# Kernel tuning notes

Hardware: AMD Instinct MI355X
Metric: run time of the kernel (lower is better)

Reference implementation:

```python
import jax, jax.numpy as jnp
import numpy as np

B, T, N_EMBD, HEAD = 4, 2048, 1024, 128


def setup_inputs() -> dict:
    key = jax.random.key(0)
    ks = jax.random.split(key, 7)
    s = 1.0 / np.sqrt(N_EMBD)
    return {
        "X": jax.random.normal(ks[0], (B, T, N_EMBD), dtype=jnp.float32),
        "Wk": jax.random.normal(ks[1], (N_EMBD, HEAD), dtype=jnp.float32) * s,
        "bk": jax.random.normal(ks[2], (HEAD,), dtype=jnp.float32) * 0.02,
        "Wq": jax.random.normal(ks[3], (N_EMBD, HEAD), dtype=jnp.float32) * s,
        "bq": jax.random.normal(ks[4], (HEAD,), dtype=jnp.float32) * 0.02,
        "Wv": jax.random.normal(ks[5], (N_EMBD, HEAD), dtype=jnp.float32) * s,
        "bv": jax.random.normal(ks[6], (HEAD,), dtype=jnp.float32) * 0.02,
    }


def reference(X, Wk, bk, Wq, bq, Wv, bv):
    # X: [B, T, C] with C = n_embd
    C = X.shape[-1]
    k = X @ Wk + bk  # [B, T, H]
    q = X @ Wq + bq  # [B, T, H]
    # NOTE: original computes k @ q^T (not q @ k^T) and scales by n_embd**-0.5.
    wei = jnp.einsum("bth,bsh->bts", k, q) * (C ** -0.5)  # [B, T, T]
    # NOTE: original's masked_fill is not in-place and its result is discarded,
    # so NO causal mask is actually applied. Dropout is identity (eval).
    wei = jax.nn.softmax(wei, axis=-1)
    v = X @ Wv + bv  # [B, T, H]
    out = jnp.einsum("bts,bsh->bth", wei, v)  # [B, T, H]
    return out
```

## Files before the change

kernel.cpp:

```cpp
#include <hip/hip_runtime.h>
#include <hip/hip_bf16.h>

#define Bn 4
#define Tn 2048
#define Cn 1024
#define Hn 128
#define Mn (Bn*Tn)
#define SCHUNKS 4
#define SCHUNK  (Tn/SCHUNKS)

typedef _Float16 f16;
typedef __attribute__((ext_vector_type(4))) _Float16 f16x4;
typedef __attribute__((ext_vector_type(8))) _Float16 f16x8;
typedef __attribute__((ext_vector_type(4))) float f32x4;

__global__ void prep_w(const float* __restrict__ Wk, const float* __restrict__ Wq,
                       const float* __restrict__ Wv, f16* __restrict__ Wt) {
    const int w = blockIdx.y;
    const float* W = (w == 0) ? Wk : (w == 1) ? Wq : Wv;
    int idx = blockIdx.x * 256 + threadIdx.x;
    int c = idx >> 7;
    int h = idx & 127;
    Wt[w * (Cn * Hn) + h * Cn + c] = (f16)W[idx];
}

__global__ __launch_bounds__(512) void qkv_gemm(const float* __restrict__ X,
                                                const f16* __restrict__ Wt,
                                                const float* __restrict__ bk,
                                                const float* __restrict__ bq,
                                                const float* __restrict__ bv,
                                                f16* __restrict__ proj) {
    __shared__ __align__(16) f16 As[32 * 72];
    __shared__ __align__(16) f16 Bs[384 * 72];

    const int tid  = threadIdx.x;
    const int r0   = blockIdx.x * 32;
    const int lane = tid & 63, wid = tid >> 6;
    const int quad = lane >> 4, l16 = lane & 15;
    const int nbase = wid * 48;

    f32x4 acc[2][3] = {};

    for (int k0 = 0; k0 < Cn; k0 += 64) {
        {
            int row = tid >> 4, c4 = tid & 15;
            float4 x = *(const float4*)(X + (r0 + row) * Cn + k0 + c4 * 4);
            f16x4 v = { (f16)x.x, (f16)x.y, (f16)x.z, (f16)x.w };
            *(f16x4*)(&As[row * 72 + c4 * 4]) = v;
        }
        for (int i = 0; i < 6; i++) {
            int ci = tid + 512 * i;
            int row = ci >> 3, cc = ci & 7;
            *(f16x8*)(&Bs[row * 72 + cc * 8]) =
                *(const f16x8*)(Wt + row * Cn + k0 + cc * 8);
        }
        __syncthreads();
        for (int ks = 0; ks < 2; ks++) {
            int kk = ks * 32;
            f16x8 af[2], bf[3];
            for (int mt = 0; mt < 2; mt++)
                af[mt] = *(const f16x8*)(&As[(mt * 16 + l16) * 72 + kk + quad * 8]);
            for (int nt = 0; nt < 3; nt++)
                bf[nt] = *(const f16x8*)(&Bs[(nbase + nt * 16 + l16) * 72 + kk + quad * 8]);
            for (int mt = 0; mt < 2; mt++)
                for (int nt = 0; nt < 3; nt++)
                    acc[mt][nt] = __builtin_amdgcn_mfma_f32_16x16x32_f16(
                        af[mt], bf[nt], acc[mt][nt], 0, 0, 0);
        }
        __syncthreads();
    }

    for (int nt = 0; nt < 3; nt++) {
        int n0 = nbase + nt * 16;
        int wsel = n0 >> 7;
        int col = (n0 & 127) + l16;
        const float* bias = (wsel == 0) ? bk : (wsel == 1) ? bq : bv;
        float bval = bias[col];
        float scale = (wsel == 0) ? 0.03125f : 1.0f;
        f16* P = proj + wsel * (Mn * Hn);
        for (int mt = 0; mt < 2; mt++)
            for (int r = 0; r < 4; r++) {
                int m = r0 + mt * 16 + quad * 4 + r;
                P[m * Hn + col] = (f16)((acc[mt][nt][r] + bval) * scale);
            }
    }
}

__global__ __launch_bounds__(256) void vt_transpose(const f16* __restrict__ pv,
                                                    f16* __restrict__ vT) {
    __shared__ __align__(16) f16 T[64 * 72];
    const int tid = threadIdx.x;
    const int s0 = blockIdx.x * 64, h0 = blockIdx.y * 64, b = blockIdx.z;
    for (int i = 0; i < 2; i++) {
        int ci = tid + 256 * i;
        int row = ci >> 3, hc = ci & 7;
        *(f16x8*)(&T[row * 72 + hc * 8]) =
            *(const f16x8*)(pv + (b * Tn + s0 + row) * Hn + h0 + hc * 8);
    }
    __syncthreads();
    for (int i = 0; i < 2; i++) {
        int ci = tid + 256 * i;
        int h = ci >> 3, sc = ci & 7;
        f16x8 v;
        for (int j = 0; j < 8; j++) v[j] = T[(sc * 8 + j) * 72 + h];
        *(f16x8*)(&vT[(b * Hn + h0 + h) * Tn + s0 + sc * 8]) = v;
    }
}

__global__ __launch_bounds__(256) void attn_kernel(const f16* __restrict__ pk,
                                                   const f16* __restrict__ pq,
                                                   const f16* __restrict__ vT,
                                                   float* __restrict__ pO,
                                                   float* __restrict__ pm,
                                                   float* __restrict__ pl) {
    __shared__ __align__(16) char smem[36864];
    f16* Bq = (f16*)smem;
    f16* Vt = (f16*)(smem + 17408);

    const int tid  = threadIdx.x;
    const int tblk = blockIdx.x, c = blockIdx.y, b = blockIdx.z;
    const int t0   = tblk * 64;
    const int lane = tid & 63, wid = tid >> 6;
    const int quad = lane >> 4, l16 = lane & 15;
    const int tg   = t0 + wid * 16 + l16;

    const f16* kp = pk + b * Tn * Hn;
    const f16* qp = pq + b * Tn * Hn;
    const f16* vp = vT + b * Hn * Tn;

    f16x8 kfr[4];
    for (int ks = 0; ks < 4; ks++)
        kfr[ks] = *(const f16x8*)(kp + tg * Hn + ks * 32 + quad * 8);

    float m_i = -3e38f, l_i = 0.0f;
    f32x4 accO[8] = {};

    for (int si = 0; si < SCHUNK / 64; si++) {
        const int s0 = c * SCHUNK + si * 64;
        for (int i = 0; i < 4; i++) {
            int ci = tid + 256 * i;
            int row = ci >> 4, hc = ci & 15;
            *(f16x8*)(&Bq[row * 136 + hc * 8]) =
                *(const f16x8*)(qp + (s0 + row) * Hn + hc * 8);
        }
        for (int i = 0; i < 4; i++) {
            int ci = tid + 256 * i;
            int h = ci >> 3, sc = ci & 7;
            *(f16x8*)(&Vt[h * 72 + sc * 8]) =
                *(const f16x8*)(vp + h * Tn + s0 + sc * 8);
        }
        __syncthreads();

        f32x4 accS[4] = {};
        for (int ks = 0; ks < 4; ks++) {
            int kk = ks * 32;
            for (int st = 0; st < 4; st++) {
                f16x8 af = *(const f16x8*)(&Bq[(st * 16 + l16) * 136 + kk + quad * 8]);
                accS[st] = __builtin_amdgcn_mfma_f32_16x16x32_f16(af, kfr[ks], accS[st], 0, 0, 0);
            }
        }

        float mloc = -3e38f;
        for (int st = 0; st < 4; st++)
            for (int r = 0; r < 4; r++) mloc = fmaxf(mloc, accS[st][r]);
        mloc = fmaxf(mloc, __shfl_xor(mloc, 16));
        mloc = fmaxf(mloc, __shfl_xor(mloc, 32));
        float mnew = fmaxf(m_i, mloc);
        float alpha = __expf(m_i - mnew);
        m_i = mnew;

        f16x4 pf[4];
        float psum = 0.0f;
        for (int st = 0; st < 4; st++) {
            f32x4 p;
            for (int r = 0; r < 4; r++) {
                p[r] = __expf(accS[st][r] - mnew);
                psum += p[r];
            }
            pf[st] = { (f16)p[0], (f16)p[1], (f16)p[2], (f16)p[3] };
        }
        psum += __shfl_xor(psum, 16);
        psum += __shfl_xor(psum, 32);
        l_i = l_i * alpha + psum;

        for (int ht = 0; ht < 8; ht++)
            for (int r = 0; r < 4; r++) accO[ht][r] *= alpha;

        for (int st = 0; st < 4; st++) {
            for (int ht = 0; ht < 8; ht++) {
                f16x4 av = *(const f16x4*)(&Vt[(ht * 16 + l16) * 72 + st * 16 + quad * 4]);
                accO[ht] = __builtin_amdgcn_mfma_f32_16x16x16f16(av, pf[st], accO[ht], 0, 0, 0);
            }
        }
        __syncthreads();
    }

    float* ep = (float*)smem + wid * 2048;
    for (int ht = 0; ht < 8; ht++)
        for (int r = 0; r < 4; r++)
            ep[(ht * 16 + quad * 4 + r) * 16 + l16] = accO[ht][r];
    __syncthreads();
    {
        int t = lane >> 2, hq = lane & 3;
        int tgl = t0 + wid * 16 + t;
        float* dst = pO + ((size_t)(c * Bn + b) * Tn + tgl) * Hn + hq * 32;
        for (int j = 0; j < 8; j++) {
            float4 v = { ep[(hq * 32 + j * 4 + 0) * 16 + t],
                         ep[(hq * 32 + j * 4 + 1) * 16 + t],
                         ep[(hq * 32 + j * 4 + 2) * 16 + t],
                         ep[(hq * 32 + j * 4 + 3) * 16 + t] };
            *(float4*)(dst + j * 4) = v;
        }
    }
    if (quad == 0) {
        pm[(c * Bn + b) * Tn + t0 + wid * 16 + l16] = m_i;
        pl[(c * Bn + b) * Tn + t0 + wid * 16 + l16] = l_i;
    }
}

__global__ __launch_bounds__(256) void merge_kernel(const float* __restrict__ pO,
                                                    const float* __restrict__ pm,
                                                    const float* __restrict__ pl,
                                                    float* __restrict__ out) {
    int gid = blockIdx.x * 256 + threadIdx.x;
    int tg = gid >> 2;
    int hq = gid & 3;
    float mc[SCHUNKS], lc[SCHUNKS];
    float M = -3e38f;
    for (int cI = 0; cI < SCHUNKS; cI++) {
        mc[cI] = pm[cI * (Bn * Tn) + tg];
        lc[cI] = pl[cI * (Bn * Tn) + tg];
        M = fmaxf(M, mc[cI]);
    }
    float L = 0.0f, wc[SCHUNKS];
    for (int cI = 0; cI < SCHUNKS; cI++) {
        wc[cI] = __expf(mc[cI] - M);
        L += wc[cI] * lc[cI];
    }
    float inv = 1.0f / L;
    float4 o[8] = {};
    for (int cI = 0; cI < SCHUNKS; cI++) {
        const float* src = pO + ((size_t)cI * Bn * Tn + tg) * Hn + hq * 32;
        float w = wc[cI];
        for (int j = 0; j < 8; j++) {
            float4 v = *(const float4*)(src + j * 4);
            o[j].x += w * v.x; o[j].y += w * v.y; o[j].z += w * v.z; o[j].w += w * v.w;
        }
    }
    float* dst = out + (size_t)tg * Hn + hq * 32;
    for (int j = 0; j < 8; j++) {
        float4 v = { o[j].x * inv, o[j].y * inv, o[j].z * inv, o[j].w * inv };
        *(float4*)(dst + j * 4) = v;
    }
}

extern "C" void kernel_launch(void* const* d_in, const int* in_sizes, int n_in,
                              void* d_out, int out_size, void* d_ws, size_t ws_size,
                              hipStream_t stream) {
    const float* X  = (const float*)d_in[0];
    const float* Wk = (const float*)d_in[1];
    const float* bk = (const float*)d_in[2];
    const float* Wq = (const float*)d_in[3];
    const float* bq = (const float*)d_in[4];
    const float* Wv = (const float*)d_in[5];
    const float* bv = (const float*)d_in[6];
    float* out = (float*)d_out;

    char* base = (char*)d_ws;
    f16*   Wt   = (f16*)(base);
    f16*   proj = (f16*)(base + 786432);
    f16*   pk   = proj;
    f16*   pq   = proj + Mn * Hn;
    f16*   pv   = proj + 2 * Mn * Hn;
    f16*   vT   = (f16*)(base + 7077888);
    float* pO   = (float*)(base + 9175040);
    float* pm   = (float*)(base + 25952256);
    float* pl   = (float*)(base + 26083328);

    prep_w<<<dim3(512, 3), 256, 0, stream>>>(Wk, Wq, Wv, Wt);
    qkv_gemm<<<dim3(Mn / 32), 512, 0, stream>>>(X, Wt, bk, bq, bv, proj);
    vt_transpose<<<dim3(Tn / 64, Hn / 64, Bn), 256, 0, stream>>>(pv, vT);
    attn_kernel<<<dim3(Tn / 64, SCHUNKS, Bn), 256, 0, stream>>>(pk, pq, vT, pO, pm, pl);
    merge_kernel<<<dim3(128), 256, 0, stream>>>(pO, pm, pl, out);
}
```

Measured before the change: 146.2 us.

## Double per-wave row tile in attention, split S into 8 chunks, store partials as fp16

```diff
diff --git a/kernel.cpp b/kernel.cpp
--- a/kernel.cpp
+++ b/kernel.cpp
@@ -6,7 +6,7 @@
 #define Cn 1024
 #define Hn 128
 #define Mn (Bn*Tn)
-#define SCHUNKS 4
+#define SCHUNKS 8
 #define SCHUNK  (Tn/SCHUNKS)
 
 typedef _Float16 f16;
@@ -107,33 +107,34 @@
     }
 }
 
-__global__ __launch_bounds__(256) void attn_kernel(const f16* __restrict__ pk,
-                                                   const f16* __restrict__ pq,
-                                                   const f16* __restrict__ vT,
-                                                   float* __restrict__ pO,
-                                                   float* __restrict__ pm,
-                                                   float* __restrict__ pl) {
+__global__ __launch_bounds__(256, 2) void attn_kernel(const f16* __restrict__ pk,
+                                                      const f16* __restrict__ pq,
+                                                      const f16* __restrict__ vT,
+                                                      f16* __restrict__ pO,
+                                                      float* __restrict__ pm,
+                                                      float* __restrict__ pl) {
     __shared__ __align__(16) char smem[36864];
     f16* Bq = (f16*)smem;
     f16* Vt = (f16*)(smem + 17408);
 
     const int tid  = threadIdx.x;
     const int tblk = blockIdx.x, c = blockIdx.y, b = blockIdx.z;
-    const int t0   = tblk * 64;
+    const int t0   = tblk * 128;
     const int lane = tid & 63, wid = tid >> 6;
     const int quad = lane >> 4, l16 = lane & 15;
-    const int tg   = t0 + wid * 16 + l16;
+    const int tw   = t0 + wid * 32;
 
     const f16* kp = pk + b * Tn * Hn;
     const f16* qp = pq + b * Tn * Hn;
     const f16* vp = vT + b * Hn * Tn;
 
-    f16x8 kfr[4];
-    for (int ks = 0; ks < 4; ks++)
-        kfr[ks] = *(const f16x8*)(kp + tg * Hn + ks * 32 + quad * 8);
-
-    float m_i = -3e38f, l_i = 0.0f;
-    f32x4 accO[8] = {};
+    f16x8 kfr[2][4];
+    for (int tt = 0; tt < 2; tt++)
+        for (int ks = 0; ks < 4; ks++)
+            kfr[tt][ks] = *(const f16x8*)(kp + (tw + tt * 16 + l16) * Hn + ks * 32 + quad * 8);
+
+    float m_i[2] = { -3e38f, -3e38f }, l_i[2] = { 0.0f, 0.0f };
+    f32x4 accO[2][8] = {};
 
     for (int si = 0; si < SCHUNK / 64; si++) {
         const int s0 = c * SCHUNK + si * 64;
@@ -151,74 +152,78 @@
         }
         __syncthreads();
 
-        f32x4 accS[4] = {};
+        f32x4 accS[2][4] = {};
         for (int ks = 0; ks < 4; ks++) {
             int kk = ks * 32;
             for (int st = 0; st < 4; st++) {
                 f16x8 af = *(const f16x8*)(&Bq[(st * 16 + l16) * 136 + kk + quad * 8]);
-                accS[st] = __builtin_amdgcn_mfma_f32_16x16x32_f16(af, kfr[ks], accS[st], 0, 0, 0);
-            }
-        }
-
-        float mloc = -3e38f;
-        for (int st = 0; st < 4; st++)
-            for (int r = 0; r < 4; r++) mloc = fmaxf(mloc, accS[st][r]);
-        mloc = fmaxf(mloc, __shfl_xor(mloc, 16));
-        mloc = fmaxf(mloc, __shfl_xor(mloc, 32));
-        float mnew = fmaxf(m_i, mloc);
-        float alpha = __expf(m_i - mnew);
-        m_i = mnew;
-
-        f16x4 pf[4];
-        float psum = 0.0f;
-        for (int st = 0; st < 4; st++) {
-            f32x4 p;
-            for (int r = 0; r < 4; r++) {
-                p[r] = __expf(accS[st][r] - mnew);
-                psum += p[r];
-            }
-            pf[st] = { (f16)p[0], (f16)p[1], (f16)p[2], (f16)p[3] };
-        }
-        psum += __shfl_xor(psum, 16);
-        psum += __shfl_xor(psum, 32);
-        l_i = l_i * alpha + psum;
-
-        for (int ht = 0; ht < 8; ht++)
-            for (int r = 0; r < 4; r++) accO[ht][r] *= alpha;
+                accS[0][st] = __builtin_amdgcn_mfma_f32_16x16x32_f16(af, kfr[0][ks], accS[0][st], 0, 0, 0);
+                accS[1][st] = __builtin_amdgcn_mfma_f32_16x16x32_f16(af, kfr[1][ks], accS[1][st], 0, 0, 0);
+            }
+        }
+
+        f16x4 pf[2][4];
+        for (int tt = 0; tt < 2; tt++) {
+            float mloc = -3e38f;
+            for (int st = 0; st < 4; st++)
+                for (int r = 0; r < 4; r++) mloc = fmaxf(mloc, accS[tt][st][r]);
+            mloc = fmaxf(mloc, __shfl_xor(mloc, 16));
+            mloc = fmaxf(mloc, __shfl_xor(mloc, 32));
+            float mnew = fmaxf(m_i[tt], mloc);
+            float alpha = __expf(m_i[tt] - mnew);
+            m_i[tt] = mnew;
+            float psum = 0.0f;
+            for (int st = 0; st < 4; st++) {
+                f32x4 p;
+                for (int r = 0; r < 4; r++) {
+                    p[r] = __expf(accS[tt][st][r] - mnew);
+                    psum += p[r];
+                }
+                pf[tt][st] = { (f16)p[0], (f16)p[1], (f16)p[2], (f16)p[3] };
+            }
+            psum += __shfl_xor(psum, 16);
+            psum += __shfl_xor(psum, 32);
+            l_i[tt] = l_i[tt] * alpha + psum;
+            for (int ht = 0; ht < 8; ht++)
+                for (int r = 0; r < 4; r++) accO[tt][ht][r] *= alpha;
+        }
 
         for (int st = 0; st < 4; st++) {
             for (int ht = 0; ht < 8; ht++) {
                 f16x4 av = *(const f16x4*)(&Vt[(ht * 16 + l16) * 72 + st * 16 + quad * 4]);
-                accO[ht] = __builtin_amdgcn_mfma_f32_16x16x16f16(av, pf[st], accO[ht], 0, 0, 0);
-            }
-        }
-        __syncthreads();
-    }
-
-    float* ep = (float*)smem + wid * 2048;
-    for (int ht = 0; ht < 8; ht++)
-        for (int r = 0; r < 4; r++)
-            ep[(ht * 16 + quad * 4 + r) * 16 + l16] = accO[ht][r];
-    __syncthreads();
-    {
-        int t = lane >> 2, hq = lane & 3;
-        int tgl = t0 + wid * 16 + t;
-        float* dst = pO + ((size_t)(c * Bn + b) * Tn + tgl) * Hn + hq * 32;
-        for (int j = 0; j < 8; j++) {
-            float4 v = { ep[(hq * 32 + j * 4 + 0) * 16 + t],
-                         ep[(hq * 32 + j * 4 + 1) * 16 + t],
-                         ep[(hq * 32 + j * 4 + 2) * 16 + t],
-                         ep[(hq * 32 + j * 4 + 3) * 16 + t] };
-            *(float4*)(dst + j * 4) = v;
-        }
-    }
-    if (quad == 0) {
-        pm[(c * Bn + b) * Tn + t0 + wid * 16 + l16] = m_i;
-        pl[(c * Bn + b) * Tn + t0 + wid * 16 + l16] = l_i;
-    }
-}
-
-__global__ __launch_bounds__(256) void merge_kernel(const float* __restrict__ pO,
+                accO[0][ht] = __builtin_amdgcn_mfma_f32_16x16x16f16(av, pf[0][st], accO[0][ht], 0, 0, 0);
+                accO[1][ht] = __builtin_amdgcn_mfma_f32_16x16x16f16(av, pf[1][st], accO[1][ht], 0, 0, 0);
+            }
+        }
+        __syncthreads();
+    }
+
+    for (int tt = 0; tt < 2; tt++) {
+        __syncthreads();
+        float* ep = (float*)smem + wid * 2048;
+        for (int ht = 0; ht < 8; ht++)
+            for (int r = 0; r < 4; r++)
+                ep[(ht * 16 + quad * 4 + r) * 16 + l16] = accO[tt][ht][r];
+        __syncthreads();
+        {
+            int t = lane >> 2, hq = lane & 3;
+            int tgl = tw + tt * 16 + t;
+            f16* dst = pO + ((size_t)(c * Bn + b) * Tn + tgl) * Hn + hq * 32;
+            for (int g = 0; g < 4; g++) {
+                f16x8 v;
+                for (int j = 0; j < 8; j++)
+                    v[j] = (f16)ep[(hq * 32 + g * 8 + j) * 16 + t];
+                *(f16x8*)(dst + g * 8) = v;
+            }
+        }
+        if (quad == 0) {
+            pm[(c * Bn + b) * Tn + tw + tt * 16 + l16] = m_i[tt];
+            pl[(c * Bn + b) * Tn + tw + tt * 16 + l16] = l_i[tt];
+        }
+    }
+}
+
+__global__ __launch_bounds__(256) void merge_kernel(const f16* __restrict__ pO,
                                                     const float* __restrict__ pm,
                                                     const float* __restrict__ pl,
                                                     float* __restrict__ out) {
@@ -238,19 +243,19 @@
         L += wc[cI] * lc[cI];
     }
     float inv = 1.0f / L;
-    float4 o[8] = {};
+    float o[32] = {};
     for (int cI = 0; cI < SCHUNKS; cI++) {
-        const float* src = pO + ((size_t)cI * Bn * Tn + tg) * Hn + hq * 32;
+        const f16* src = pO + ((size_t)cI * Bn * Tn + tg) * Hn + hq * 32;
         float w = wc[cI];
-        for (int j = 0; j < 8; j++) {
-            float4 v = *(const float4*)(src + j * 4);
-            o[j].x += w * v.x; o[j].y += w * v.y; o[j].z += w * v.z; o[j].w += w * v.w;
+        for (int g = 0; g < 4; g++) {
+            f16x8 v = *(const f16x8*)(src + g * 8);
+            for (int j = 0; j < 8; j++) o[g * 8 + j] += w * (float)v[j];
         }
     }
     float* dst = out + (size_t)tg * Hn + hq * 32;
-    for (int j = 0; j < 8; j++) {
-        float4 v = { o[j].x * inv, o[j].y * inv, o[j].z * inv, o[j].w * inv };
-        *(float4*)(dst + j * 4) = v;
+    for (int g = 0; g < 8; g++) {
+        float4 v = { o[g*4+0] * inv, o[g*4+1] * inv, o[g*4+2] * inv, o[g*4+3] * inv };
+        *(float4*)(dst + g * 4) = v;
     }
 }
 
@@ -273,13 +278,13 @@
     f16*   pq   = proj + Mn * Hn;
     f16*   pv   = proj + 2 * Mn * Hn;
     f16*   vT   = (f16*)(base + 7077888);
-    float* pO   = (float*)(base + 9175040);
+    f16*   pO   = (f16*)(base + 9175040);
     float* pm   = (float*)(base + 25952256);
-    float* pl   = (float*)(base + 26083328);
+    float* pl   = (float*)(base + 26214400);
 
     prep_w<<<dim3(512, 3), 256, 0, stream>>>(Wk, Wq, Wv, Wt);
     qkv_gemm<<<dim3(Mn / 32), 512, 0, stream>>>(X, Wt, bk, bq, bv, proj);
     vt_transpose<<<dim3(Tn / 64, Hn / 64, Bn), 256, 0, stream>>>(pv, vT);
-    attn_kernel<<<dim3(Tn / 64, SCHUNKS, Bn), 256, 0, stream>>>(pk, pq, vT, pO, pm, pl);
+    attn_kernel<<<dim3(Tn / 128, SCHUNKS, Bn), 256, 0, stream>>>(pk, pq, vT, pO, pm, pl);
     merge_kernel<<<dim3(128), 256, 0, stream>>>(pO, pm, pl, out);
 }
```

After: 136.4 us. 6.7% less time.
